# Optimization experiments

Measured on AMD Instinct MI355X. Metric: run time of the kernel, lower is better.

The kernel has to match this reference:

```python
import jax, jax.numpy as jnp
import numpy as np

NUM_GROUPS = 32
EPS = 1e-6


def setup_inputs() -> dict:
    key = jax.random.key(0)
    ks = jax.random.split(key, 10)
    B, C, L = 8, 512, 4096
    s = 1.0 / np.sqrt(C)
    x = jax.random.normal(ks[0], (B, C, L), dtype=jnp.float32)
    gn_w = jnp.ones((C,), jnp.float32)
    gn_b = jnp.zeros((C,), jnp.float32)
    wq = jax.random.normal(ks[1], (C, C), jnp.float32) * s
    bq = jax.random.normal(ks[2], (C,), jnp.float32) * 0.01
    wk = jax.random.normal(ks[3], (C, C), jnp.float32) * s
    bk = jax.random.normal(ks[4], (C,), jnp.float32) * 0.01
    wv = jax.random.normal(ks[5], (C, C), jnp.float32) * s
    bv = jax.random.normal(ks[6], (C,), jnp.float32) * 0.01
    wo = jax.random.normal(ks[7], (C, C), jnp.float32) * s
    bo = jax.random.normal(ks[8], (C,), jnp.float32) * 0.01
    return {"x": x, "gn_w": gn_w, "gn_b": gn_b, "wq": wq, "bq": bq,
            "wk": wk, "bk": bk, "wv": wv, "bv": bv, "wo": wo, "bo": bo}


def _group_norm(x, w, b):
    # x: [B, C, L]; normalize over each group's (C/G, L) slice
    B, C, L = x.shape
    g = x.reshape(B, NUM_GROUPS, C // NUM_GROUPS, L)
    mu = jnp.mean(g, axis=(2, 3), keepdims=True)
    var = jnp.var(g, axis=(2, 3), keepdims=True)
    g = (g - mu) * jax.lax.rsqrt(var + EPS)
    return g.reshape(B, C, L) * w[None, :, None] + b[None, :, None]


def _conv1x1(h, w, b):
    # pointwise conv: [B,C,L] x [Cout,Cin] -> [B,Cout,L]
    return jnp.einsum('oc,bcl->bol', w, h) + b[None, :, None]


def reference(x, gn_w, gn_b, wq, bq, wk, bk, wv, bv, wo, bo):
    h = _group_norm(x, gn_w, gn_b)
    q = _conv1x1(h, wq, bq)
    k = _conv1x1(h, wk, bk)
    v = _conv1x1(h, wv, bv)
    B, C, L = q.shape
    scale = jnp.asarray(C, q.dtype) ** -0.5
    # w_[b,i,j] = sum_c q[b,c,i] k[b,c,j]
    w_ = jnp.einsum('bci,bcj->bij', q, k) * scale
    w_ = jax.nn.softmax(w_, axis=2)
    # h[b,c,i] = sum_j v[b,c,j] w_[b,i,j]
    h = jnp.einsum('bcj,bij->bci', v, w_)
    return x + _conv1x1(h, wo, bo)
```

## Files before the change

kernel.cpp:

```cpp
#include <hip/hip_runtime.h>
#include <hip/hip_bf16.h>
#include <math.h>

#define DI __device__ __forceinline__

typedef unsigned short u16;
typedef unsigned int   u32;
typedef unsigned long long u64;
typedef __attribute__((ext_vector_type(8))) short short8;
typedef __attribute__((ext_vector_type(4))) float f32x4;

constexpr int CB = 512;
constexpr int LL = 4096;
constexpr int NG = 32;

DI float bf2f(u16 u) { u32 v = ((u32)u) << 16; float f; __builtin_memcpy(&f, &v, 4); return f; }
DI u16 f2bf(float f) {
  u32 u; __builtin_memcpy(&u, &f, 4);
  u += 0x7fffu + ((u >> 16) & 1u);
  return (u16)(u >> 16);
}

DI void gload16(const void* g, void* l) {
  __builtin_amdgcn_global_load_lds((const __attribute__((address_space(1))) u32*)g,
                                   (__attribute__((address_space(3))) u32*)l, 16, 0, 0);
}

__global__ __launch_bounds__(256) void conv_w(
    const float* __restrict__ wq, const float* __restrict__ wk,
    const float* __restrict__ wv, const float* __restrict__ wo,
    const float* __restrict__ bq, const float* __restrict__ bk,
    const float* __restrict__ bv,
    u16* __restrict__ wqkv, u16* __restrict__ wob, float* __restrict__ bqkv) {
  if (blockIdx.x < 1024) {
    int i = blockIdx.x * 256 + threadIdx.x;
    wqkv[i]          = f2bf(wq[i]);
    wqkv[262144 + i] = f2bf(wk[i]);
    wqkv[524288 + i] = f2bf(wv[i]);
    wob[i]           = f2bf(wo[i]);
  } else {
    for (int j = 0; j < 6; ++j) {
      int idx = j * 256 + threadIdx.x;
      float b = (idx < 512) ? bq[idx] : (idx < 1024) ? bk[idx - 512] : bv[idx - 1024];
      bqkv[idx] = b;
    }
  }
}

__global__ __launch_bounds__(256) void gn_stats(const float* __restrict__ x,
                                                float* __restrict__ stats) {
  const float4* base = (const float4*)(x + (long)blockIdx.x * (16 * LL));
  float s = 0.f, ss = 0.f;
  for (int i = threadIdx.x; i < 16 * LL / 4; i += 256) {
    float4 v = base[i];
    s  += v.x + v.y + v.z + v.w;
    ss += v.x * v.x + v.y * v.y + v.z * v.z + v.w * v.w;
  }
#pragma unroll
  for (int o = 32; o; o >>= 1) { s += __shfl_xor(s, o); ss += __shfl_xor(ss, o); }
  __shared__ float red[8];
  int wv = threadIdx.x >> 6, ln = threadIdx.x & 63;
  if (ln == 0) { red[wv * 2] = s; red[wv * 2 + 1] = ss; }
  __syncthreads();
  if (threadIdx.x == 0) {
    float S = red[0] + red[2] + red[4] + red[6];
    float SS = red[1] + red[3] + red[5] + red[7];
    float mu = S * (1.f / 65536.f);
    float var = SS * (1.f / 65536.f) - mu * mu;
    stats[blockIdx.x * 2]     = mu;
    stats[blockIdx.x * 2 + 1] = rsqrtf(var + 1e-6f);
  }
}

__global__ __launch_bounds__(256) void gn_apply(
    const float* __restrict__ x, const float* __restrict__ gw,
    const float* __restrict__ gb, const float* __restrict__ stats,
    u16* __restrict__ hT) {
  __shared__ u16 t[64][66];
  const int b = blockIdx.z, c0 = blockIdx.y * 64, l0 = blockIdx.x * 64;
  const int ln = threadIdx.x & 63, sub = threadIdx.x >> 6;
  for (int cr = sub; cr < 64; cr += 4) {
    int c = c0 + cr;
    float v  = x[(long)b * CB * LL + (long)c * LL + l0 + ln];
    float mu = stats[(b * NG + (c >> 4)) * 2];
    float rs = stats[(b * NG + (c >> 4)) * 2 + 1];
    t[cr][ln] = f2bf((v - mu) * rs * gw[c] + gb[c]);
  }
  __syncthreads();
  for (int lr = sub; lr < 64; lr += 4)
    hT[(long)b * LL * CB + (long)(l0 + lr) * CB + c0 + ln] = t[ln][lr];
}

template <int BM, int BN, int EPI, bool SWZ, int WR, int WC>
__global__ __launch_bounds__(WR * WC * 64) void gemm_bt(
    const u16* __restrict__ A, int lda, long asb,
    const u16* __restrict__ Bt, int ldb, long bsb,
    int K, const float* __restrict__ bias, float scale,
    u16* __restrict__ o0, u16* __restrict__ o1, u16* __restrict__ o2,
    float* __restrict__ of, const float* __restrict__ xres, long osb, int ldo) {
  constexpr int NT = WR * WC * 64;
  constexpr int FM = BM / WR / 16, FN = BN / WC / 16;
  static_assert((BM * 8) % NT == 0 && (BN * 8) % NT == 0, "staging div");
  __shared__ u16 smem[(BM + BN) * 64];
  u16* lA = smem;
  u16* lB = smem + BM * 64;

  int bx = blockIdx.x, by = blockIdx.y;
  if constexpr (SWZ) {
    const int nwg = gridDim.x * gridDim.y;
    const int id = by * gridDim.x + bx;
    const int id2 = (id & 7) * (nwg >> 3) + (id >> 3);
    bx = id2 % gridDim.x;
    by = id2 / gridDim.x;
  }

  const int tid = threadIdx.x;
  const int lane = tid & 63;
  const int wv = tid >> 6;
  const int wr = wv / WC, wc = wv % WC;
  const int fr = lane & 15, fq = lane >> 4;
  const int bz = blockIdx.z;
  const int bzb  = (EPI == 4) ? (bz >> 1) : bz;
  const int kbeg = (EPI == 4) ? (bz & 1) * K : 0;

  const u16* Ab = A + (long)bzb * asb + (long)(by * BM) * lda;
  const u16* Bb = Bt + (long)bzb * bsb + (long)(bx * BN) * ldb;

  f32x4 acc[FM][FN];
#pragma unroll
  for (int m = 0; m < FM; ++m)
#pragma unroll
    for (int n = 0; n < FN; ++n) acc[m][n] = (f32x4)(0.f);

  for (int k0 = kbeg; k0 < kbeg + K; k0 += 64) {
#pragma unroll
    for (int p = 0; p < BM * 8 / NT; ++p) {
      int t = p * NT + tid;
      int row = t >> 3;
      int cbl = ((t & 7) << 4) ^ ((row & 7) << 4);
      gload16(Ab + (long)row * lda + k0 + (cbl >> 1), &lA[t * 8]);
    }
#pragma unroll
    for (int p = 0; p < BN * 8 / NT; ++p) {
      int t = p * NT + tid;
      int row = t >> 3;
      int cbl = ((t & 7) << 4) ^ ((row & 7) << 4);
      gload16(Bb + (long)row * ldb + k0 + (cbl >> 1), &lB[t * 8]);
    }
    __syncthreads();
#pragma unroll
    for (int ks = 0; ks < 2; ++ks) {
      short8 af[FM], bfr[FN];
#pragma unroll
      for (int m = 0; m < FM; ++m) {
        int row = wr * (BM / WR) + m * 16 + fr;
        int cb = (ks * 64 + fq * 16) ^ ((row & 7) << 4);
        af[m] = *(const short8*)((const char*)lA + row * 128 + cb);
      }
#pragma unroll
      for (int n = 0; n < FN; ++n) {
        int row = wc * (BN / WC) + n * 16 + fr;
        int cb = (ks * 64 + fq * 16) ^ ((row & 7) << 4);
        bfr[n] = *(const short8*)((const char*)lB + row * 128 + cb);
      }
#pragma unroll
      for (int m = 0; m < FM; ++m)
#pragma unroll
        for (int n = 0; n < FN; ++n)
          acc[m][n] = __builtin_amdgcn_mfma_f32_16x16x32_bf16(af[m], bfr[n], acc[m][n], 0, 0, 0);
    }
    __syncthreads();
  }

  const int ml0 = wr * (BM / WR);
  const int nl0 = wc * (BN / WC);

  if constexpr (EPI == 3) {
    const int mg0 = by * BM + ml0;
    const int ng0 = bx * BN + nl0;
#pragma unroll
    for (int m = 0; m < FM; ++m)
#pragma unroll
      for (int n = 0; n < FN; ++n) {
        const int ng = ng0 + n * 16 + fr;
#pragma unroll
        for (int r = 0; r < 4; ++r) {
          const int mg = mg0 + m * 16 + fq * 4 + r;
          const long off = (long)bz * osb + (long)mg * ldo + ng;
          of[off] = acc[m][n][r] + bias[mg] + xres[off];
        }
      }
  } else if constexpr (EPI == 0) {
    const int mat = (by * BM) >> 9;
    if (mat < 2) {
#pragma unroll
      for (int m = 0; m < FM; ++m)
#pragma unroll
        for (int n = 0; n < FN; ++n) {
          const int nl = nl0 + n * 16 + fr;
#pragma unroll
          for (int r = 0; r < 4; ++r) {
            const int ml = ml0 + m * 16 + fq * 4 + r;
            smem[nl * BM + (ml ^ ((nl & 7) << 3))] =
                f2bf(acc[m][n][r] + bias[by * BM + ml]);
          }
        }
      __syncthreads();
      u16* dst0 = (mat == 0 ? o0 : o1) + (long)bz * ((long)LL * CB) +
                  (long)(bx * BN) * CB + ((by * BM) & 511);
      for (int i = tid * 8; i < BM * BN; i += NT * 8) {
        const int rr = i / BM, cc = i % BM;
        short8 val = *(const short8*)&smem[rr * BM + (cc ^ ((rr & 7) << 3))];
        *(short8*)(dst0 + (long)rr * CB + cc) = val;
      }
    } else {
#pragma unroll
      for (int m = 0; m < FM; ++m)
#pragma unroll
        for (int n = 0; n < FN; ++n) {
          const int nl = nl0 + n * 16 + fr;
#pragma unroll
          for (int r = 0; r < 4; ++r) {
            const int ml = ml0 + m * 16 + fq * 4 + r;
            smem[ml * BN + (nl ^ ((ml & 7) << 3))] =
                f2bf(acc[m][n][r] + bias[by * BM + ml]);
          }
        }
      __syncthreads();
      u16* dst0 = o2 + (long)bz * ((long)CB * LL) +
                  (long)((by * BM) & 511) * LL + bx * BN;
      for (int i = tid * 8; i < BM * BN; i += NT * 8) {
        const int rr = i / BN, cc = i % BN;
        short8 val = *(const short8*)&smem[rr * BN + (cc ^ ((rr & 7) << 3))];
        *(short8*)(dst0 + (long)rr * LL + cc) = val;
      }
    }
  } else if constexpr (EPI == 4) {
    const float* rls = xres + (long)(bz >> 1) * LL + by * BM;
#pragma unroll
    for (int m = 0; m < FM; ++m)
#pragma unroll
      for (int n = 0; n < FN; ++n) {
        const int nl = nl0 + n * 16 + fr;
#pragma unroll
        for (int r = 0; r < 4; ++r) {
          const int ml = ml0 + m * 16 + fq * 4 + r;
          smem[ml * BN + (nl ^ ((ml & 7) << 3))] = f2bf(acc[m][n][r] * rls[ml]);
        }
      }
    __syncthreads();
    u16* dst0 = ((bz & 1) ? o1 : o0) + (long)(bz >> 1) * ((long)LL * CB) +
                (long)(by * BM) * ldo + bx * BN;
    for (int i = tid * 8; i < BM * BN; i += NT * 8) {
      const int rr = i / BN, cc = i % BN;
      short8 val = *(const short8*)&smem[rr * BN + (cc ^ ((rr & 7) << 3))];
      *(short8*)(dst0 + (long)rr * ldo + cc) = val;
    }
  } else {
#pragma unroll
    for (int m = 0; m < FM; ++m)
#pragma unroll
      for (int n = 0; n < FN; ++n) {
        const int nl = nl0 + n * 16 + fr;
#pragma unroll
        for (int r = 0; r < 4; ++r) {
          const int ml = ml0 + m * 16 + fq * 4 + r;
          smem[ml * BN + (nl ^ ((ml & 7) << 3))] = f2bf(exp2f(acc[m][n][r] * scale));
        }
      }
    __syncthreads();
    u16* dst0 = o0 + (long)bz * osb + (long)(by * BM) * ldo + bx * BN;
    for (int i = tid * 8; i < BM * BN; i += NT * 8) {
      const int rr = i / BN, cc = i % BN;
      short8 val = *(const short8*)&smem[rr * BN + (cc ^ ((rr & 7) << 3))];
      *(short8*)(dst0 + (long)rr * ldo + cc) = val;
    }
  }
}

__global__ __launch_bounds__(256) void rsum_rows(const u16* __restrict__ S,
                                                 float* __restrict__ rls) {
  const u16* row = S + ((long)blockIdx.y * LL + blockIdx.x) * LL;
  const int tid = threadIdx.x;
  const int wv = tid >> 6, ln = tid & 63;
  short8 a = ((const short8*)row)[tid * 2];
  short8 b = ((const short8*)row)[tid * 2 + 1];
  float s = 0.f;
#pragma unroll
  for (int j = 0; j < 8; ++j) s += bf2f((u16)a[j]) + bf2f((u16)b[j]);
#pragma unroll
  for (int o = 32; o; o >>= 1) s += __shfl_xor(s, o);
  __shared__ float red[4];
  if (ln == 0) red[wv] = s;
  __syncthreads();
  if (tid == 0)
    rls[(long)blockIdx.y * LL + blockIdx.x] =
        1.0f / (red[0] + red[1] + red[2] + red[3]);
}

__global__ __launch_bounds__(256) void reduce_pp(
    const u16* __restrict__ p0, const u16* __restrict__ p1, u16* __restrict__ o) {
  const long base = (long)blockIdx.y * ((long)LL * CB) +
                    (long)(blockIdx.x * 256 + threadIdx.x) * 16;
#pragma unroll
  for (int h = 0; h < 2; ++h) {
    short8 a = *(const short8*)(p0 + base + h * 8);
    short8 b = *(const short8*)(p1 + base + h * 8);
    short8 r;
#pragma unroll
    for (int j = 0; j < 8; ++j)
      r[j] = (short)f2bf(bf2f((u16)a[j]) + bf2f((u16)b[j]));
    *(short8*)(o + base + h * 8) = r;
  }
}

extern "C" void kernel_launch(void* const* d_in, const int* in_sizes, int n_in,
                              void* d_out, int out_size, void* d_ws, size_t ws_size,
                              hipStream_t stream) {
  const float* x   = (const float*)d_in[0];
  const float* gnw = (const float*)d_in[1];
  const float* gnb = (const float*)d_in[2];
  const float* wq  = (const float*)d_in[3];
  const float* bq  = (const float*)d_in[4];
  const float* wk  = (const float*)d_in[5];
  const float* bk  = (const float*)d_in[6];
  const float* wv  = (const float*)d_in[7];
  const float* bv  = (const float*)d_in[8];
  const float* wo  = (const float*)d_in[9];
  const float* bo  = (const float*)d_in[10];
  float* out = (float*)d_out;

  char* ws = (char*)d_ws;
  const long NEL = (long)LL * CB;
  const long SEL = (long)LL * LL;
  float* stats = (float*)ws;
  float* bqkv  = (float*)(ws + 8192);
  u16* wqkv = (u16*)(ws + 16384);
  u16* wob  = (u16*)(ws + 16384 + 1572864);
  float* rlsm = (float*)(ws + (3l << 20));
  u16* hT   = (u16*)(ws + (4l << 20));
  u16* qT   = hT + 8 * NEL;
  u16* kT   = qT + 8 * NEL;
  u16* vN   = kT + 8 * NEL;
  const size_t base = (4ul << 20) + 4ul * 8 * NEL * 2;

  int G;
  u16 *Sbuf, *aT;
  if (ws_size >= base + 2ul * SEL * 2) G = 2;
  else                                 G = 1;
  if (G > 1) { Sbuf = (u16*)(ws + base); aT = hT; }
  else       { Sbuf = hT; aT = qT; }

  conv_w<<<1025, 256, 0, stream>>>(wq, wk, wv, wo, bq, bk, bv, wqkv, wob, bqkv);
  gn_stats<<<256, 256, 0, stream>>>(x, stats);
  gn_apply<<<dim3(64, 8, 8), 256, 0, stream>>>(x, gnw, gnb, stats, hT);

  gemm_bt<128, 128, 0, false, 2, 2><<<dim3(32, 12, 8), 256, 0, stream>>>(
      wqkv, 512, 0, hT, 512, NEL, 512, bqkv, 1.f, qT, kT, vN, nullptr, nullptr, 0, 0);

  const float cl = (1.0f / sqrtf(512.0f)) * 1.44269504f;
  for (int g0 = 0; g0 < 8; g0 += G) {
    gemm_bt<128, 128, 1, false, 2, 2><<<dim3(32, 32, G), 256, 0, stream>>>(
        qT + (long)g0 * NEL, 512, NEL, kT + (long)g0 * NEL, 512, NEL, 512,
        nullptr, cl, Sbuf, nullptr, nullptr, nullptr, nullptr, SEL, LL);
    rsum_rows<<<dim3(LL, G), 256, 0, stream>>>(Sbuf, rlsm);
    gemm_bt<128, 128, 4, true, 2, 4><<<dim3(4, 32, 2 * G), 512, 0, stream>>>(
        Sbuf, LL, SEL, vN + (long)g0 * NEL, LL, NEL, 2048,
        nullptr, 1.f, qT + (long)g0 * NEL, kT + (long)g0 * NEL, nullptr,
        nullptr, rlsm, 0, CB);
    reduce_pp<<<dim3(512, G), 256, 0, stream>>>(
        qT + (long)g0 * NEL, kT + (long)g0 * NEL, aT + (long)g0 * NEL);
  }

  gemm_bt<128, 128, 3, false, 2, 2><<<dim3(32, 4, 8), 256, 0, stream>>>(
      wob, 512, 0, aT, 512, NEL, 512, bo, 1.f,
      nullptr, nullptr, nullptr, out, x, NEL, LL);

  (void)in_sizes; (void)n_in; (void)out_size; (void)ws_size;
}
```

Measured before the change: 627.6 us.

## Add 256x256 ping-pong pipelined GEMM for QKV projection and QK^T scores

Introduces a new 512-thread GEMM kernel with 256x256 tiles, double-buffered LDS staging through global_load_lds, and interleaved LDS reads and MFMA quarters separated by barriers and priority hints. It replaces the 128x128 gemm_bt for the QKV projection and the QK^T exp-score stages, and the now-unused epilogues are removed from gemm_bt. The aim is to raise operand reuse per tile and overlap global loads with MFMA work. In exchange it uses 128KB of LDS per block and many accumulator registers, which can limit occupancy and leaves fewer blocks per launch.

```diff
diff --git a/kernel.cpp b/kernel.cpp
--- a/kernel.cpp
+++ b/kernel.cpp
@@ -91,6 +91,202 @@
     hT[(long)b * LL * CB + (long)(l0 + lr) * CB + c0 + ln] = t[ln][lr];
 }
 
+template <int Q>
+DI void rdA(const u16* LB, int wr, int fr, int fq, short8 af[2][2]) {
+#pragma unroll
+  for (int m2 = 0; m2 < 2; ++m2)
+#pragma unroll
+    for (int kk = 0; kk < 2; ++kk) {
+      const int R = wr * 128 + (Q * 2 + m2) * 16 + fr;
+      af[m2][kk] = *(const short8*)((const char*)LB + R * 128 +
+                                    ((kk * 64 + fq * 16) ^ ((R & 7) << 4)));
+    }
+}
+DI void rdB(const u16* LB, int wc, int fr, int fq, short8 bf[4][2]) {
+#pragma unroll
+  for (int nf = 0; nf < 4; ++nf)
+#pragma unroll
+    for (int kk = 0; kk < 2; ++kk) {
+      const int R = wc * 64 + nf * 16 + fr;
+      bf[nf][kk] = *(const short8*)((const char*)LB + R * 128 +
+                                    ((kk * 64 + fq * 16) ^ ((R & 7) << 4)));
+    }
+}
+template <int Q>
+DI void mmaQ(short8 af[2][2], short8 bf[4][2], f32x4 acc[8][4]) {
+#pragma unroll
+  for (int kk = 0; kk < 2; ++kk)
+#pragma unroll
+    for (int m2 = 0; m2 < 2; ++m2)
+#pragma unroll
+      for (int nf = 0; nf < 4; ++nf)
+        acc[Q * 2 + m2][nf] = __builtin_amdgcn_mfma_f32_16x16x32_bf16(
+            af[m2][kk], bf[nf][kk], acc[Q * 2 + m2][nf], 0, 0, 0);
+}
+
+#define PTAIL(Q)                                             \
+  __builtin_amdgcn_s_barrier();                              \
+  asm volatile("s_waitcnt lgkmcnt(0)" ::: "memory");         \
+  __builtin_amdgcn_sched_barrier(0);                         \
+  __builtin_amdgcn_s_setprio(1);                             \
+  mmaQ<Q>(af, bf, acc);                                      \
+  __builtin_amdgcn_s_setprio(0);                             \
+  __builtin_amdgcn_s_barrier();
+
+template <int EPI>
+__global__ __launch_bounds__(512, 2) void gemm8p(
+    const u16* __restrict__ A, int lda, long asb,
+    const u16* __restrict__ Bt, int ldb, long bsb,
+    int K, const float* __restrict__ bias, float scale,
+    u16* __restrict__ o0, u16* __restrict__ o1, u16* __restrict__ o2,
+    long osb, int ldo) {
+  __shared__ u16 smem[65536];
+  u16* lA0 = smem;
+  u16* lA1 = smem + 16384;
+  u16* lB0 = smem + 32768;
+  u16* lB1 = smem + 49152;
+
+  const int tid = threadIdx.x;
+  const int lane = tid & 63, wv = tid >> 6;
+  const int wr = wv >> 2, wc = wv & 3;
+  const int fr = lane & 15, fq = lane >> 4;
+  const int bx = blockIdx.x, by = blockIdx.y, bz = blockIdx.z;
+
+  const u16* Ab = A + (long)bz * asb + (long)(by * 256) * lda;
+  const u16* Bb = Bt + (long)bz * bsb + (long)(bx * 256) * ldb;
+
+  auto stage = [&](u16* lbase, const u16* gbase, int ld_, int half, int t) {
+#pragma unroll
+    for (int p = 0; p < 2; ++p) {
+      int i = p * 512 + tid;
+      int row = i >> 3, ch = i & 7;
+      int src = t * 64 + ((((ch << 4) ^ ((row & 7) << 4))) >> 1);
+      gload16(gbase + (long)(half * 128 + row) * ld_ + src,
+              lbase + half * 8192 + i * 8);
+    }
+  };
+
+  f32x4 acc[8][4];
+#pragma unroll
+  for (int m = 0; m < 8; ++m)
+#pragma unroll
+    for (int n = 0; n < 4; ++n) acc[m][n] = (f32x4)(0.f);
+
+  stage(lA0, Ab, lda, 0, 0); stage(lA0, Ab, lda, 1, 0);
+  stage(lB0, Bb, ldb, 0, 0); stage(lB0, Bb, ldb, 1, 0);
+  stage(lB1, Bb, ldb, 0, 1); stage(lB1, Bb, ldb, 1, 1);
+  asm volatile("s_waitcnt vmcnt(4)" ::: "memory");
+  __builtin_amdgcn_sched_barrier(0);
+  __builtin_amdgcn_s_barrier();
+
+  const int nt = K >> 6;
+  short8 af[2][2], bf[4][2];
+  for (int i = 0; i < nt / 2; ++i) {
+    const bool last = (i == nt / 2 - 1);
+    const int t1 = 2 * i + 1, t2 = 2 * i + 2, t3 = 2 * i + 3;
+    rdB(lB0, wc, fr, fq, bf);
+    rdA<0>(lA0, wr, fr, fq, af);
+    stage(lA1, Ab, lda, 0, t1);
+    PTAIL(0)
+    rdA<1>(lA0, wr, fr, fq, af);
+    stage(lA1, Ab, lda, 1, t1);
+    PTAIL(1)
+    rdA<2>(lA0, wr, fr, fq, af);
+    if (!last) stage(lB0, Bb, ldb, 0, t2);
+    PTAIL(2)
+    rdA<3>(lA0, wr, fr, fq, af);
+    if (!last) stage(lB0, Bb, ldb, 1, t2);
+    if (last) { asm volatile("s_waitcnt vmcnt(0)" ::: "memory"); }
+    else      { asm volatile("s_waitcnt vmcnt(4)" ::: "memory"); }
+    __builtin_amdgcn_sched_barrier(0);
+    PTAIL(3)
+    rdB(lB1, wc, fr, fq, bf);
+    rdA<0>(lA1, wr, fr, fq, af);
+    if (!last) stage(lA0, Ab, lda, 0, t2);
+    PTAIL(0)
+    rdA<1>(lA1, wr, fr, fq, af);
+    if (!last) stage(lA0, Ab, lda, 1, t2);
+    PTAIL(1)
+    rdA<2>(lA1, wr, fr, fq, af);
+    if (!last) stage(lB1, Bb, ldb, 0, t3);
+    PTAIL(2)
+    rdA<3>(lA1, wr, fr, fq, af);
+    if (!last) stage(lB1, Bb, ldb, 1, t3);
+    if (!last) {
+      asm volatile("s_waitcnt vmcnt(4)" ::: "memory");
+      __builtin_amdgcn_sched_barrier(0);
+    }
+    PTAIL(3)
+  }
+
+  if constexpr (EPI == 1) {
+#pragma unroll
+    for (int mf = 0; mf < 8; ++mf)
+#pragma unroll
+      for (int nf = 0; nf < 4; ++nf) {
+        const int nl = wc * 64 + nf * 16 + fr;
+#pragma unroll
+        for (int r = 0; r < 4; ++r) {
+          const int ml = wr * 128 + mf * 16 + fq * 4 + r;
+          smem[ml * 256 + (nl ^ ((ml & 7) << 3))] =
+              f2bf(exp2f(acc[mf][nf][r] * scale));
+        }
+      }
+    __syncthreads();
+    u16* dst0 = o0 + (long)bz * osb + (long)(by * 256) * ldo + bx * 256;
+    for (int i = tid * 8; i < 65536; i += 4096) {
+      const int rr = i >> 8, cc = i & 255;
+      short8 val = *(const short8*)&smem[rr * 256 + (cc ^ ((rr & 7) << 3))];
+      *(short8*)(dst0 + (long)rr * ldo + cc) = val;
+    }
+  } else {
+    const int mat = by >> 1;
+    if (mat < 2) {
+#pragma unroll
+      for (int mf = 0; mf < 8; ++mf)
+#pragma unroll
+        for (int nf = 0; nf < 4; ++nf) {
+          const int nl = wc * 64 + nf * 16 + fr;
+#pragma unroll
+          for (int r = 0; r < 4; ++r) {
+            const int ml = wr * 128 + mf * 16 + fq * 4 + r;
+            smem[nl * 256 + (ml ^ ((nl & 7) << 3))] =
+                f2bf(acc[mf][nf][r] + bias[by * 256 + ml]);
+          }
+        }
+      __syncthreads();
+      u16* dst0 = (mat == 0 ? o0 : o1) + (long)bz * ((long)LL * CB) +
+                  (long)(bx * 256) * CB + ((by * 256) & 511);
+      for (int i = tid * 8; i < 65536; i += 4096) {
+        const int rr = i >> 8, cc = i & 255;
+        short8 val = *(const short8*)&smem[rr * 256 + (cc ^ ((rr & 7) << 3))];
+        *(short8*)(dst0 + (long)rr * CB + cc) = val;
+      }
+    } else {
+#pragma unroll
+      for (int mf = 0; mf < 8; ++mf)
+#pragma unroll
+        for (int nf = 0; nf < 4; ++nf) {
+          const int nl = wc * 64 + nf * 16 + fr;
+#pragma unroll
+          for (int r = 0; r < 4; ++r) {
+            const int ml = wr * 128 + mf * 16 + fq * 4 + r;
+            smem[ml * 256 + (nl ^ ((ml & 7) << 3))] =
+                f2bf(acc[mf][nf][r] + bias[by * 256 + ml]);
+          }
+        }
+      __syncthreads();
+      u16* dst0 = o2 + (long)bz * ((long)CB * LL) +
+                  (long)((by * 256) & 511) * LL + bx * 256;
+      for (int i = tid * 8; i < 65536; i += 4096) {
+        const int rr = i >> 8, cc = i & 255;
+        short8 val = *(const short8*)&smem[rr * 256 + (cc ^ ((rr & 7) << 3))];
+        *(short8*)(dst0 + (long)rr * LL + cc) = val;
+      }
+    }
+  }
+}
+
 template <int BM, int BN, int EPI, bool SWZ, int WR, int WC>
 __global__ __launch_bounds__(WR * WC * 64) void gemm_bt(
     const u16* __restrict__ A, int lda, long asb,
@@ -190,52 +386,7 @@
           of[off] = acc[m][n][r] + bias[mg] + xres[off];
         }
       }
-  } else if constexpr (EPI == 0) {
-    const int mat = (by * BM) >> 9;
-    if (mat < 2) {
-#pragma unroll
-      for (int m = 0; m < FM; ++m)
-#pragma unroll
-        for (int n = 0; n < FN; ++n) {
-          const int nl = nl0 + n * 16 + fr;
-#pragma unroll
-          for (int r = 0; r < 4; ++r) {
-            const int ml = ml0 + m * 16 + fq * 4 + r;
-            smem[nl * BM + (ml ^ ((nl & 7) << 3))] =
-                f2bf(acc[m][n][r] + bias[by * BM + ml]);
-          }
-        }
-      __syncthreads();
-      u16* dst0 = (mat == 0 ? o0 : o1) + (long)bz * ((long)LL * CB) +
-                  (long)(bx * BN) * CB + ((by * BM) & 511);
-      for (int i = tid * 8; i < BM * BN; i += NT * 8) {
-        const int rr = i / BM, cc = i % BM;
-        short8 val = *(const short8*)&smem[rr * BM + (cc ^ ((rr & 7) << 3))];
-        *(short8*)(dst0 + (long)rr * CB + cc) = val;
-      }
-    } else {
-#pragma unroll
-      for (int m = 0; m < FM; ++m)
-#pragma unroll
-        for (int n = 0; n < FN; ++n) {
-          const int nl = nl0 + n * 16 + fr;
-#pragma unroll
-          for (int r = 0; r < 4; ++r) {
-            const int ml = ml0 + m * 16 + fq * 4 + r;
-            smem[ml * BN + (nl ^ ((ml & 7) << 3))] =
-                f2bf(acc[m][n][r] + bias[by * BM + ml]);
-          }
-        }
-      __syncthreads();
-      u16* dst0 = o2 + (long)bz * ((long)CB * LL) +
-                  (long)((by * BM) & 511) * LL + bx * BN;
-      for (int i = tid * 8; i < BM * BN; i += NT * 8) {
-        const int rr = i / BN, cc = i % BN;
-        short8 val = *(const short8*)&smem[rr * BN + (cc ^ ((rr & 7) << 3))];
-        *(short8*)(dst0 + (long)rr * LL + cc) = val;
-      }
-    }
-  } else if constexpr (EPI == 4) {
+  } else {
     const float* rls = xres + (long)(bz >> 1) * LL + by * BM;
 #pragma unroll
     for (int m = 0; m < FM; ++m)
@@ -251,25 +402,6 @@
     __syncthreads();
     u16* dst0 = ((bz & 1) ? o1 : o0) + (long)(bz >> 1) * ((long)LL * CB) +
                 (long)(by * BM) * ldo + bx * BN;
-    for (int i = tid * 8; i < BM * BN; i += NT * 8) {
-      const int rr = i / BN, cc = i % BN;
-      short8 val = *(const short8*)&smem[rr * BN + (cc ^ ((rr & 7) << 3))];
-      *(short8*)(dst0 + (long)rr * ldo + cc) = val;
-    }
-  } else {
-#pragma unroll
-    for (int m = 0; m < FM; ++m)
-#pragma unroll
-      for (int n = 0; n < FN; ++n) {
-        const int nl = nl0 + n * 16 + fr;
-#pragma unroll
-        for (int r = 0; r < 4; ++r) {
-          const int ml = ml0 + m * 16 + fq * 4 + r;
-          smem[ml * BN + (nl ^ ((ml & 7) << 3))] = f2bf(exp2f(acc[m][n][r] * scale));
-        }
-      }
-    __syncthreads();
-    u16* dst0 = o0 + (long)bz * osb + (long)(by * BM) * ldo + bx * BN;
     for (int i = tid * 8; i < BM * BN; i += NT * 8) {
       const int rr = i / BN, cc = i % BN;
       short8 val = *(const short8*)&smem[rr * BN + (cc ^ ((rr & 7) << 3))];
@@ -355,14 +487,14 @@
   gn_stats<<<256, 256, 0, stream>>>(x, stats);
   gn_apply<<<dim3(64, 8, 8), 256, 0, stream>>>(x, gnw, gnb, stats, hT);
 
-  gemm_bt<128, 128, 0, false, 2, 2><<<dim3(32, 12, 8), 256, 0, stream>>>(
-      wqkv, 512, 0, hT, 512, NEL, 512, bqkv, 1.f, qT, kT, vN, nullptr, nullptr, 0, 0);
+  gemm8p<0><<<dim3(16, 6, 8), 512, 0, stream>>>(
+      wqkv, 512, 0, hT, 512, NEL, 512, bqkv, 1.f, qT, kT, vN, 0, 0);
 
   const float cl = (1.0f / sqrtf(512.0f)) * 1.44269504f;
   for (int g0 = 0; g0 < 8; g0 += G) {
-    gemm_bt<128, 128, 1, false, 2, 2><<<dim3(32, 32, G), 256, 0, stream>>>(
+    gemm8p<1><<<dim3(16, 16, G), 512, 0, stream>>>(
         qT + (long)g0 * NEL, 512, NEL, kT + (long)g0 * NEL, 512, NEL, 512,
-        nullptr, cl, Sbuf, nullptr, nullptr, nullptr, nullptr, SEL, LL);
+        nullptr, cl, Sbuf, nullptr, nullptr, SEL, LL);
     rsum_rows<<<dim3(LL, G), 256, 0, stream>>>(Sbuf, rlsm);
     gemm_bt<128, 128, 4, true, 2, 4><<<dim3(4, 32, 2 * G), 512, 0, stream>>>(
         Sbuf, LL, SEL, vN + (long)g0 * NEL, LL, NEL, 2048,
```

After: 619.0 us. About the same (-1.4%).
